# Kernel optimization log

Hardware: AMD Instinct MI355X
Metric: run time of the kernel (lower is better)

The kernel has to match this reference:

```python
import jax, jax.numpy as jnp
import numpy as np

B, S, D = 4, 2048, 1024
H, Dh = 16, 64


def setup_inputs() -> dict:
    key = jax.random.key(0)
    ks = jax.random.split(key, 9)
    s_in = 1.0 / np.sqrt(D)
    inp = {
        "key": jax.random.normal(ks[0], (B, S, D), jnp.float32),
        "value": jax.random.normal(ks[1], (B, S, D), jnp.float32),
        "query": jax.random.normal(ks[2], (B, S, D), jnp.float32),
        # Linear weights stored as [in, out] (math-equivalent to torch W.T)
        "Wq": jax.random.uniform(ks[3], (D, H * Dh), jnp.float32, -s_in, s_in),
        "bq": jax.random.uniform(ks[4], (H * Dh,), jnp.float32, -s_in, s_in),
        "Wk": jax.random.uniform(ks[5], (D, H * Dh), jnp.float32, -s_in, s_in),
        "bk": jax.random.uniform(ks[6], (H * Dh,), jnp.float32, -s_in, s_in),
        "Wv": jax.random.uniform(ks[7], (D, H * Dh), jnp.float32, -s_in, s_in),
        "bv": jax.random.uniform(ks[8], (H * Dh,), jnp.float32, -s_in, s_in),
    }
    return inp


def reference(key, value, query, Wq, bq, Wk, bk, Wv, bv):
    b, s, _ = key.shape
    # projections -> [B, H, S, Dh]
    q = (query @ Wq + bq).reshape(b, s, H, Dh).transpose(0, 2, 1, 3)
    k = (key @ Wk + bk).reshape(b, s, H, Dh).transpose(0, 2, 1, 3)
    v = (value @ Wv + bv).reshape(b, s, H, Dh).transpose(0, 2, 1, 3)
    scores = jnp.einsum("bhqd,bhkd->bhqk", q, k) / np.sqrt(Dh).astype(np.float32)
    p = jax.nn.softmax(scores, axis=-1)
    out = jnp.einsum("bhqk,bhkd->bhqd", p, v)  # [B, H, S, Dh]
    return out.transpose(0, 2, 1, 3).reshape(b, s, H * Dh)
```

## Files before the change

### kernel.cpp

```cpp
#include <hip/hip_runtime.h>

typedef __bf16 bf16;
typedef __bf16 bf16x8 __attribute__((ext_vector_type(8)));
typedef __bf16 bf16x4 __attribute__((ext_vector_type(4)));
typedef _Float16 f16x4 __attribute__((ext_vector_type(4)));
typedef _Float16 f16x8 __attribute__((ext_vector_type(8)));
typedef float  f32x4  __attribute__((ext_vector_type(4)));

#define LOG2E 1.44269504088896340736f

__device__ __forceinline__ void async16(const void* g, void* l) {
  __builtin_amdgcn_global_load_lds(
      (const __attribute__((address_space(1))) unsigned int*)g,
      (__attribute__((address_space(3))) unsigned int*)l, 16, 0, 0);
}

__device__ __forceinline__ f32x4 mfma_bf16(bf16x8 a, bf16x8 b, f32x4 c) {
  return __builtin_amdgcn_mfma_f32_16x16x32_bf16(a, b, c, 0, 0, 0);
}
__device__ __forceinline__ f32x4 mfma_f16k16(f16x4 a, f16x4 b, f32x4 c) {
  return __builtin_amdgcn_mfma_f32_16x16x16f16(a, b, c, 0, 0, 0);
}

__global__ __launch_bounds__(256) void cvt_f32_bf16(const float* __restrict__ in,
                                                    bf16* __restrict__ out) {
  int i = blockIdx.x * 256 + threadIdx.x;
  const float4* p = (const float4*)in;
  float4 a = p[i * 2], c = p[i * 2 + 1];
  bf16x8 r;
  r[0] = (bf16)a.x; r[1] = (bf16)a.y; r[2] = (bf16)a.z; r[3] = (bf16)a.w;
  r[4] = (bf16)c.x; r[5] = (bf16)c.y; r[6] = (bf16)c.z; r[7] = (bf16)c.w;
  ((bf16x8*)out)[i] = r;
}

__global__ __launch_bounds__(256) void wtrans(const float* __restrict__ W0,
                                              const float* __restrict__ W1,
                                              const float* __restrict__ W2,
                                              bf16* __restrict__ Wt) {
  const float* W = blockIdx.z == 0 ? W0 : (blockIdx.z == 1 ? W1 : W2);
  bf16* O = Wt + (size_t)blockIdx.z * (1024 * 1024);
  __shared__ float t[64 * 69];
  int tid = threadIdx.x;
  int k0 = blockIdx.x * 64, n0 = blockIdx.y * 64;
  int r0 = tid >> 4, c0 = (tid & 15) * 4;
#pragma unroll
  for (int rr = 0; rr < 4; rr++) {
    int k = r0 + rr * 16;
    float4 v = *(const float4*)(W + (k0 + k) * 1024 + n0 + c0);
    t[k * 69 + c0 + 0] = v.x; t[k * 69 + c0 + 1] = v.y;
    t[k * 69 + c0 + 2] = v.z; t[k * 69 + c0 + 3] = v.w;
  }
  __syncthreads();
#pragma unroll
  for (int rr = 0; rr < 4; rr++) {
    int n = r0 + rr * 16;
    bf16x4 o;
#pragma unroll
    for (int j = 0; j < 4; j++) o[j] = (bf16)t[(c0 + j) * 69 + n];
    *(bf16x4*)(O + (n0 + n) * 1024 + k0 + c0) = o;
  }
}

__global__ __launch_bounds__(256) void gemm_proj(const bf16* __restrict__ A,
                                                 const bf16* __restrict__ Bt,
                                                 const float* __restrict__ bias,
                                                 bf16* __restrict__ OutN,
                                                 _Float16* __restrict__ OutT,
                                                 int transV) {
  __shared__ bf16 smem[16384];
  bf16* sA = smem;
  bf16* sB = smem + 8192;
  const int tid = threadIdx.x;
  const int wave = tid >> 6, lane = tid & 63;
  const int quad = lane >> 4, l15 = lane & 15;
  const int m0 = blockIdx.x * 128, n0 = blockIdx.y * 128;

  const bf16* ap[4]; const bf16* bp[4]; int lo[4];
#pragma unroll
  for (int i = 0; i < 4; i++) {
    int g = wave * 256 + i * 64 + lane;
    int row = g >> 3, jl = (g & 7) ^ (row & 7);
    ap[i] = A + (m0 + row) * 1024 + jl * 8;
    bp[i] = Bt + (n0 + row) * 1024 + jl * 8;
    lo[i] = (wave * 256 + i * 64) * 8;
  }
  const int wm = (wave & 1) * 64, wn = (wave >> 1) * 64;
  f32x4 acc[4][4] = {};

  for (int kt = 0; kt < 16; kt++) {
    const int ko = kt * 64;
#pragma unroll
    for (int i = 0; i < 4; i++) async16(ap[i] + ko, sA + lo[i]);
#pragma unroll
    for (int i = 0; i < 4; i++) async16(bp[i] + ko, sB + lo[i]);
    __syncthreads();
#pragma unroll
    for (int ks = 0; ks < 2; ks++) {
      bf16x8 af[4], bv[4];
#pragma unroll
      for (int mt = 0; mt < 4; mt++) {
        int m = wm + mt * 16 + l15;
        int ph = (ks * 4 + quad) ^ (m & 7);
        af[mt] = *(const bf16x8*)(sA + m * 64 + ph * 8);
      }
#pragma unroll
      for (int nt = 0; nt < 4; nt++) {
        int n = wn + nt * 16 + l15;
        int ph = (ks * 4 + quad) ^ (n & 7);
        bv[nt] = *(const bf16x8*)(sB + n * 64 + ph * 8);
      }
#pragma unroll
      for (int mt = 0; mt < 4; mt++)
#pragma unroll
        for (int nt = 0; nt < 4; nt++)
          acc[mt][nt] = mfma_bf16(af[mt], bv[nt], acc[mt][nt]);
    }
    __syncthreads();
  }

  if (!transV) {
#pragma unroll
    for (int nt = 0; nt < 4; nt++) {
      int n = n0 + wn + nt * 16 + l15;
      float bc = bias[n];
#pragma unroll
      for (int mt = 0; mt < 4; mt++)
#pragma unroll
        for (int r = 0; r < 4; r++) {
          int m = m0 + wm + mt * 16 + quad * 4 + r;
          OutN[m * 1024 + n] = (bf16)(acc[mt][nt][r] + bc);
        }
    }
  } else {
    _Float16* sT = (_Float16*)smem;
    const int b = m0 >> 11, s0 = m0 & 2047;
    for (int half_ = 0; half_ < 2; half_++) {
      __syncthreads();
      if ((wave & 1) == half_) {
#pragma unroll
        for (int nt = 0; nt < 4; nt++) {
          int nl = wn + nt * 16 + l15;
          float bc = bias[n0 + nl];
#pragma unroll
          for (int mt = 0; mt < 4; mt++) {
            f16x4 pk;
#pragma unroll
            for (int r = 0; r < 4; r++) pk[r] = (_Float16)(acc[mt][nt][r] + bc);
            *(f16x4*)(sT + nl * 72 + mt * 16 + quad * 4) = pk;
          }
        }
      }
      __syncthreads();
      int nl = tid >> 1, mc = (tid & 1) * 32;
      int ng = n0 + nl, hh = ng >> 6, d = ng & 63;
      int base = ((b * 16 + hh) * 64 + d) * 2048 + s0 + half_ * 64 + mc;
#pragma unroll
      for (int j = 0; j < 4; j++) {
        f16x8 v = *(const f16x8*)(sT + nl * 72 + mc + j * 8);
        *(f16x8*)(OutT + base + j * 8) = v;
      }
    }
  }
}

__global__ __launch_bounds__(256) void attn(const bf16* __restrict__ Q,
                                            const bf16* __restrict__ K,
                                            const _Float16* __restrict__ Vt,
                                            float* __restrict__ Out) {
  __shared__ bf16 sQ[8192];
  __shared__ bf16 sK[4096];
  __shared__ _Float16 sV[4096];
  const int tid = threadIdx.x;
  const int wave = tid >> 6, lane = tid & 63;
  const int quad = lane >> 4, l15 = lane & 15;
  const int q0 = blockIdx.x * 128, h = blockIdx.y, b = blockIdx.z;
  const float SC = 0.125f * LOG2E;
  const bf16* Kbase = K + b * 2048 * 1024 + h * 64;
  const _Float16* Vbase = Vt + ((b * 16 + h) * 64) * 2048;

#pragma unroll
  for (int i = 0; i < 4; i++) {
    int g = i * 256 + tid;
    int row = g >> 3, jl = (g & 7) ^ (row & 7);
    async16(Q + (b * 2048 + q0 + row) * 1024 + h * 64 + jl * 8, sQ + g * 8);
  }
#pragma unroll
  for (int i = 0; i < 2; i++) {
    int g = i * 256 + tid;
    int row = g >> 3, jl = (g & 7) ^ (row & 7);
    async16(Kbase + row * 1024 + jl * 8, sK + g * 8);
    async16(Vbase + row * 2048 + jl * 8, sV + g * 8);
  }
  __syncthreads();

  bf16x8 qf[2][2];
#pragma unroll
  for (int qt2 = 0; qt2 < 2; qt2++)
#pragma unroll
    for (int ks = 0; ks < 2; ks++) {
      int m = wave * 32 + qt2 * 16 + l15;
      int ph = (ks * 4 + quad) ^ (m & 7);
      qf[qt2][ks] = *(const bf16x8*)(sQ + m * 64 + ph * 8);
    }

  f32x4 oaccT[2][4] = {};
  float ls[2] = {0.f, 0.f};

  for (int kv = 0; kv < 2048; kv += 64) {
#pragma unroll
    for (int t = 0; t < 4; t++) {
      int row = t * 16 + l15;
      bf16x8 kf0 = *(const bf16x8*)(sK + row * 64 + ((0 + quad) ^ (row & 7)) * 8);
      bf16x8 kf1 = *(const bf16x8*)(sK + row * 64 + ((4 + quad) ^ (row & 7)) * 8);
      f32x4 st0 = {}, st1 = {};
      st0 = mfma_bf16(kf0, qf[0][0], st0);
      st0 = mfma_bf16(kf1, qf[0][1], st0);
      st1 = mfma_bf16(kf0, qf[1][0], st1);
      st1 = mfma_bf16(kf1, qf[1][1], st1);
      f16x4 pf0, pf1;
#pragma unroll
      for (int r = 0; r < 4; r++) {
        float p0 = __builtin_amdgcn_exp2f(st0[r] * SC);
        float p1 = __builtin_amdgcn_exp2f(st1[r] * SC);
        ls[0] += p0; ls[1] += p1;
        pf0[r] = (_Float16)p0; pf1[r] = (_Float16)p1;
      }
      int gk = t * 2 + (quad >> 1), ofs = (quad & 1) * 4;
#pragma unroll
      for (int dt = 0; dt < 4; dt++) {
        int d = dt * 16 + l15;
        f16x4 va = *(const f16x4*)(sV + d * 64 + (gk ^ (d & 7)) * 8 + ofs);
        oaccT[0][dt] = mfma_f16k16(va, pf0, oaccT[0][dt]);
        oaccT[1][dt] = mfma_f16k16(va, pf1, oaccT[1][dt]);
      }
    }
    __syncthreads();
    if (kv + 64 < 2048) {
      int kn = kv + 64;
#pragma unroll
      for (int i = 0; i < 2; i++) {
        int g = i * 256 + tid;
        int row = g >> 3, jl = (g & 7) ^ (row & 7);
        async16(Kbase + (kn + row) * 1024 + jl * 8, sK + g * 8);
        async16(Vbase + row * 2048 + kn + jl * 8, sV + g * 8);
      }
      __syncthreads();
    }
  }

#pragma unroll
  for (int qt2 = 0; qt2 < 2; qt2++) {
    float l = ls[qt2];
    l += __shfl_xor(l, 16);
    l += __shfl_xor(l, 32);
    float inv = 1.f / l;
    int qrow = b * 2048 + q0 + wave * 32 + qt2 * 16 + l15;
#pragma unroll
    for (int dt = 0; dt < 4; dt++) {
      float4 v;
      v.x = oaccT[qt2][dt][0] * inv;
      v.y = oaccT[qt2][dt][1] * inv;
      v.z = oaccT[qt2][dt][2] * inv;
      v.w = oaccT[qt2][dt][3] * inv;
      *(float4*)(Out + qrow * 1024 + h * 64 + dt * 16 + quad * 4) = v;
    }
  }
}

extern "C" void kernel_launch(void* const* d_in, const int* in_sizes, int n_in,
                              void* d_out, int out_size, void* d_ws, size_t ws_size,
                              hipStream_t stream) {
  const float* key   = (const float*)d_in[0];
  const float* value = (const float*)d_in[1];
  const float* query = (const float*)d_in[2];
  const float* Wq = (const float*)d_in[3];
  const float* bq = (const float*)d_in[4];
  const float* Wk = (const float*)d_in[5];
  const float* bk = (const float*)d_in[6];
  const float* Wv = (const float*)d_in[7];
  const float* bv = (const float*)d_in[8];
  float* out = (float*)d_out;

  char* ws = (char*)d_ws;
  bf16* actb = (bf16*)(ws);
  bf16* wt   = (bf16*)(ws + 16777216);
  bf16* qo   = (bf16*)(ws + 16777216 + 6291456);
  bf16* ko   = (bf16*)(ws + 16777216 + 6291456 + 16777216);
  _Float16* vt = (_Float16*)(ws + 16777216 + 6291456 + 33554432);
  (void)in_sizes; (void)n_in; (void)out_size; (void)ws_size;

  wtrans<<<dim3(16, 16, 3), 256, 0, stream>>>(Wq, Wk, Wv, wt);

  cvt_f32_bf16<<<4096, 256, 0, stream>>>(query, actb);
  gemm_proj<<<dim3(64, 8), 256, 0, stream>>>(actb, wt, bq, qo, (_Float16*)nullptr, 0);

  cvt_f32_bf16<<<4096, 256, 0, stream>>>(key, actb);
  gemm_proj<<<dim3(64, 8), 256, 0, stream>>>(actb, wt + 1048576, bk, ko, (_Float16*)nullptr, 0);

  cvt_f32_bf16<<<4096, 256, 0, stream>>>(value, actb);
  gemm_proj<<<dim3(64, 8), 256, 0, stream>>>(actb, wt + 2097152, bv, (bf16*)nullptr, vt, 1);

  attn<<<dim3(16, 16, 4), 256, 0, stream>>>(qo, ko, vt, out);
}
```

Before: 331.0 us.

## Batch QKV projections, pre-swizzle V fragments, fold softmax scale, double-buffer attention loads

```diff
diff --git a/kernel.cpp b/kernel.cpp
--- a/kernel.cpp
+++ b/kernel.cpp
@@ -4,10 +4,10 @@
 typedef __bf16 bf16x8 __attribute__((ext_vector_type(8)));
 typedef __bf16 bf16x4 __attribute__((ext_vector_type(4)));
 typedef _Float16 f16x4 __attribute__((ext_vector_type(4)));
-typedef _Float16 f16x8 __attribute__((ext_vector_type(8)));
 typedef float  f32x4  __attribute__((ext_vector_type(4)));
 
 #define LOG2E 1.44269504088896340736f
+#define SCQ (0.125f * LOG2E)
 
 __device__ __forceinline__ void async16(const void* g, void* l) {
   __builtin_amdgcn_global_load_lds(
@@ -22,15 +22,20 @@
   return __builtin_amdgcn_mfma_f32_16x16x16f16(a, b, c, 0, 0, 0);
 }
 
-__global__ __launch_bounds__(256) void cvt_f32_bf16(const float* __restrict__ in,
-                                                    bf16* __restrict__ out) {
+__global__ __launch_bounds__(256) void cvt3(const float* __restrict__ q,
+                                            const float* __restrict__ k,
+                                            const float* __restrict__ v,
+                                            bf16* __restrict__ out) {
+  int z = blockIdx.y;
+  const float* in = z == 0 ? q : (z == 1 ? k : v);
+  bf16* o = out + (size_t)z * 8388608;
   int i = blockIdx.x * 256 + threadIdx.x;
   const float4* p = (const float4*)in;
   float4 a = p[i * 2], c = p[i * 2 + 1];
   bf16x8 r;
   r[0] = (bf16)a.x; r[1] = (bf16)a.y; r[2] = (bf16)a.z; r[3] = (bf16)a.w;
   r[4] = (bf16)c.x; r[5] = (bf16)c.y; r[6] = (bf16)c.z; r[7] = (bf16)c.w;
-  ((bf16x8*)out)[i] = r;
+  ((bf16x8*)o)[i] = r;
 }
 
 __global__ __launch_bounds__(256) void wtrans(const float* __restrict__ W0,
@@ -61,19 +66,25 @@
   }
 }
 
-__global__ __launch_bounds__(256) void gemm_proj(const bf16* __restrict__ A,
-                                                 const bf16* __restrict__ Bt,
-                                                 const float* __restrict__ bias,
-                                                 bf16* __restrict__ OutN,
-                                                 _Float16* __restrict__ OutT,
-                                                 int transV) {
+__global__ __launch_bounds__(256) void gemm_qkv(const bf16* __restrict__ Act,
+                                                const bf16* __restrict__ Wt,
+                                                const float* __restrict__ b0,
+                                                const float* __restrict__ b1,
+                                                const float* __restrict__ b2,
+                                                bf16* __restrict__ qo,
+                                                bf16* __restrict__ ko,
+                                                _Float16* __restrict__ vf) {
   __shared__ bf16 smem[16384];
   bf16* sA = smem;
   bf16* sB = smem + 8192;
   const int tid = threadIdx.x;
   const int wave = tid >> 6, lane = tid & 63;
   const int quad = lane >> 4, l15 = lane & 15;
+  const int z = blockIdx.z;
   const int m0 = blockIdx.x * 128, n0 = blockIdx.y * 128;
+  const bf16* A = Act + (size_t)z * 8388608;
+  const bf16* Bt = Wt + (size_t)z * 1048576;
+  const float* bias = z == 0 ? b0 : (z == 1 ? b1 : b2);
 
   const bf16* ap[4]; const bf16* bp[4]; int lo[4];
 #pragma unroll
@@ -88,11 +99,11 @@
   f32x4 acc[4][4] = {};
 
   for (int kt = 0; kt < 16; kt++) {
-    const int ko = kt * 64;
-#pragma unroll
-    for (int i = 0; i < 4; i++) async16(ap[i] + ko, sA + lo[i]);
-#pragma unroll
-    for (int i = 0; i < 4; i++) async16(bp[i] + ko, sB + lo[i]);
+    const int ko_ = kt * 64;
+#pragma unroll
+    for (int i = 0; i < 4; i++) async16(ap[i] + ko_, sA + lo[i]);
+#pragma unroll
+    for (int i = 0; i < 4; i++) async16(bp[i] + ko_, sB + lo[i]);
     __syncthreads();
 #pragma unroll
     for (int ks = 0; ks < 2; ks++) {
@@ -118,7 +129,9 @@
     __syncthreads();
   }
 
-  if (!transV) {
+  if (z != 2) {
+    bf16* O = z == 0 ? qo : ko;
+    const float sc = z == 0 ? SCQ : 1.0f;
 #pragma unroll
     for (int nt = 0; nt < 4; nt++) {
       int n = n0 + wn + nt * 16 + l15;
@@ -128,36 +141,24 @@
 #pragma unroll
         for (int r = 0; r < 4; r++) {
           int m = m0 + wm + mt * 16 + quad * 4 + r;
-          OutN[m * 1024 + n] = (bf16)(acc[mt][nt][r] + bc);
+          O[m * 1024 + n] = (bf16)((acc[mt][nt][r] + bc) * sc);
         }
     }
   } else {
-    _Float16* sT = (_Float16*)smem;
     const int b = m0 >> 11, s0 = m0 & 2047;
-    for (int half_ = 0; half_ < 2; half_++) {
-      __syncthreads();
-      if ((wave & 1) == half_) {
-#pragma unroll
-        for (int nt = 0; nt < 4; nt++) {
-          int nl = wn + nt * 16 + l15;
-          float bc = bias[n0 + nl];
-#pragma unroll
-          for (int mt = 0; mt < 4; mt++) {
-            f16x4 pk;
-#pragma unroll
-            for (int r = 0; r < 4; r++) pk[r] = (_Float16)(acc[mt][nt][r] + bc);
-            *(f16x4*)(sT + nl * 72 + mt * 16 + quad * 4) = pk;
-          }
-        }
-      }
-      __syncthreads();
-      int nl = tid >> 1, mc = (tid & 1) * 32;
-      int ng = n0 + nl, hh = ng >> 6, d = ng & 63;
-      int base = ((b * 16 + hh) * 64 + d) * 2048 + s0 + half_ * 64 + mc;
-#pragma unroll
-      for (int j = 0; j < 4; j++) {
-        f16x8 v = *(const f16x8*)(sT + nl * 72 + mc + j * 8);
-        *(f16x8*)(OutT + base + j * 8) = v;
+    const int kvb = (s0 + wm) >> 6;
+#pragma unroll
+    for (int nt = 0; nt < 4; nt++) {
+      int nn = n0 + wn + nt * 16;
+      int h = nn >> 6, dt = (nn >> 4) & 3;
+      float bc = bias[nn + l15];
+#pragma unroll
+      for (int mt = 0; mt < 4; mt++) {
+        f16x4 pk;
+#pragma unroll
+        for (int r = 0; r < 4; r++) pk[r] = (_Float16)(acc[mt][nt][r] + bc);
+        size_t off = ((((size_t)(b * 16 + h) * 32 + kvb) * 16 + (mt * 4 + dt)) * 64 + lane) * 4;
+        *(f16x4*)(vf + off) = pk;
       }
     }
   }
@@ -165,31 +166,30 @@
 
 __global__ __launch_bounds__(256) void attn(const bf16* __restrict__ Q,
                                             const bf16* __restrict__ K,
-                                            const _Float16* __restrict__ Vt,
+                                            const _Float16* __restrict__ VF,
                                             float* __restrict__ Out) {
   __shared__ bf16 sQ[8192];
-  __shared__ bf16 sK[4096];
-  __shared__ _Float16 sV[4096];
+  __shared__ bf16 sK[2][4096];
+  __shared__ _Float16 sV[2][4096];
   const int tid = threadIdx.x;
   const int wave = tid >> 6, lane = tid & 63;
   const int quad = lane >> 4, l15 = lane & 15;
   const int q0 = blockIdx.x * 128, h = blockIdx.y, b = blockIdx.z;
-  const float SC = 0.125f * LOG2E;
-  const bf16* Kbase = K + b * 2048 * 1024 + h * 64;
-  const _Float16* Vbase = Vt + ((b * 16 + h) * 64) * 2048;
+  const bf16* Kbase = K + (size_t)(b * 2048) * 1024 + h * 64;
+  const _Float16* Vbase = VF + (size_t)(b * 16 + h) * 131072;
 
 #pragma unroll
   for (int i = 0; i < 4; i++) {
     int g = i * 256 + tid;
     int row = g >> 3, jl = (g & 7) ^ (row & 7);
-    async16(Q + (b * 2048 + q0 + row) * 1024 + h * 64 + jl * 8, sQ + g * 8);
+    async16(Q + (size_t)(b * 2048 + q0 + row) * 1024 + h * 64 + jl * 8, sQ + g * 8);
   }
 #pragma unroll
   for (int i = 0; i < 2; i++) {
     int g = i * 256 + tid;
     int row = g >> 3, jl = (g & 7) ^ (row & 7);
-    async16(Kbase + row * 1024 + jl * 8, sK + g * 8);
-    async16(Vbase + row * 2048 + jl * 8, sV + g * 8);
+    async16(Kbase + row * 1024 + jl * 8, sK[0] + g * 8);
+    async16(Vbase + g * 8, sV[0] + g * 8);
   }
   __syncthreads();
 
@@ -199,19 +199,34 @@
 #pragma unroll
     for (int ks = 0; ks < 2; ks++) {
       int m = wave * 32 + qt2 * 16 + l15;
-      int ph = (ks * 4 + quad) ^ (m & 7);
+      int ph = (ks * 4 + quad) ^ (l15 & 7);
       qf[qt2][ks] = *(const bf16x8*)(sQ + m * 64 + ph * 8);
     }
 
   f32x4 oaccT[2][4] = {};
   float ls[2] = {0.f, 0.f};
 
-  for (int kv = 0; kv < 2048; kv += 64) {
+  const int ph0 = quad ^ (l15 & 7), ph1 = (4 + quad) ^ (l15 & 7);
+
+  for (int kvb = 0; kvb < 32; kvb++) {
+    const int cur = kvb & 1;
+    if (kvb < 31) {
+      int kn = (kvb + 1) * 64;
+#pragma unroll
+      for (int i = 0; i < 2; i++) {
+        int g = i * 256 + tid;
+        int row = g >> 3, jl = (g & 7) ^ (row & 7);
+        async16(Kbase + (size_t)(kn + row) * 1024 + jl * 8, sK[cur ^ 1] + g * 8);
+        async16(Vbase + (kvb + 1) * 4096 + g * 8, sV[cur ^ 1] + g * 8);
+      }
+    }
+    const bf16* sKc = sK[cur];
+    const _Float16* sVc = sV[cur];
 #pragma unroll
     for (int t = 0; t < 4; t++) {
       int row = t * 16 + l15;
-      bf16x8 kf0 = *(const bf16x8*)(sK + row * 64 + ((0 + quad) ^ (row & 7)) * 8);
-      bf16x8 kf1 = *(const bf16x8*)(sK + row * 64 + ((4 + quad) ^ (row & 7)) * 8);
+      bf16x8 kf0 = *(const bf16x8*)(sKc + row * 64 + ph0 * 8);
+      bf16x8 kf1 = *(const bf16x8*)(sKc + row * 64 + ph1 * 8);
       f32x4 st0 = {}, st1 = {};
       st0 = mfma_bf16(kf0, qf[0][0], st0);
       st0 = mfma_bf16(kf1, qf[0][1], st0);
@@ -220,32 +235,19 @@
       f16x4 pf0, pf1;
 #pragma unroll
       for (int r = 0; r < 4; r++) {
-        float p0 = __builtin_amdgcn_exp2f(st0[r] * SC);
-        float p1 = __builtin_amdgcn_exp2f(st1[r] * SC);
+        float p0 = __builtin_amdgcn_exp2f(st0[r]);
+        float p1 = __builtin_amdgcn_exp2f(st1[r]);
         ls[0] += p0; ls[1] += p1;
         pf0[r] = (_Float16)p0; pf1[r] = (_Float16)p1;
       }
-      int gk = t * 2 + (quad >> 1), ofs = (quad & 1) * 4;
 #pragma unroll
       for (int dt = 0; dt < 4; dt++) {
-        int d = dt * 16 + l15;
-        f16x4 va = *(const f16x4*)(sV + d * 64 + (gk ^ (d & 7)) * 8 + ofs);
+        f16x4 va = *(const f16x4*)(sVc + ((t * 4 + dt) * 64 + lane) * 4);
         oaccT[0][dt] = mfma_f16k16(va, pf0, oaccT[0][dt]);
         oaccT[1][dt] = mfma_f16k16(va, pf1, oaccT[1][dt]);
       }
     }
     __syncthreads();
-    if (kv + 64 < 2048) {
-      int kn = kv + 64;
-#pragma unroll
-      for (int i = 0; i < 2; i++) {
-        int g = i * 256 + tid;
-        int row = g >> 3, jl = (g & 7) ^ (row & 7);
-        async16(Kbase + (kn + row) * 1024 + jl * 8, sK + g * 8);
-        async16(Vbase + row * 2048 + kn + jl * 8, sV + g * 8);
-      }
-      __syncthreads();
-    }
   }
 
 #pragma unroll
@@ -262,7 +264,7 @@
       v.y = oaccT[qt2][dt][1] * inv;
       v.z = oaccT[qt2][dt][2] * inv;
       v.w = oaccT[qt2][dt][3] * inv;
-      *(float4*)(Out + qrow * 1024 + h * 64 + dt * 16 + quad * 4) = v;
+      *(float4*)(Out + (size_t)qrow * 1024 + h * 64 + dt * 16 + quad * 4) = v;
     }
   }
 }
@@ -282,23 +284,15 @@
   float* out = (float*)d_out;
 
   char* ws = (char*)d_ws;
-  bf16* actb = (bf16*)(ws);
-  bf16* wt   = (bf16*)(ws + 16777216);
-  bf16* qo   = (bf16*)(ws + 16777216 + 6291456);
-  bf16* ko   = (bf16*)(ws + 16777216 + 6291456 + 16777216);
-  _Float16* vt = (_Float16*)(ws + 16777216 + 6291456 + 33554432);
+  bf16* actb   = (bf16*)(ws);
+  bf16* wt     = (bf16*)(ws + 50331648);
+  bf16* qo     = (bf16*)(ws + 56623104);
+  bf16* ko     = (bf16*)(ws + 73400320);
+  _Float16* vf = (_Float16*)(ws + 90177536);
   (void)in_sizes; (void)n_in; (void)out_size; (void)ws_size;
 
   wtrans<<<dim3(16, 16, 3), 256, 0, stream>>>(Wq, Wk, Wv, wt);
-
-  cvt_f32_bf16<<<4096, 256, 0, stream>>>(query, actb);
-  gemm_proj<<<dim3(64, 8), 256, 0, stream>>>(actb, wt, bq, qo, (_Float16*)nullptr, 0);
-
-  cvt_f32_bf16<<<4096, 256, 0, stream>>>(key, actb);
-  gemm_proj<<<dim3(64, 8), 256, 0, stream>>>(actb, wt + 1048576, bk, ko, (_Float16*)nullptr, 0);
-
-  cvt_f32_bf16<<<4096, 256, 0, stream>>>(value, actb);
-  gemm_proj<<<dim3(64, 8), 256, 0, stream>>>(actb, wt + 2097152, bv, (bf16*)nullptr, vt, 1);
-
-  attn<<<dim3(16, 16, 4), 256, 0, stream>>>(qo, ko, vt, out);
-}
+  cvt3<<<dim3(4096, 3), 256, 0, stream>>>(query, key, value, actb);
+  gemm_qkv<<<dim3(64, 8, 3), 256, 0, stream>>>(actb, wt, bq, bk, bv, qo, ko, vf);
+  attn<<<dim3(16, 16, 4), 256, 0, stream>>>(qo, ko, vf, out);
+}
```

Measured after the change: 335.6 us. About the same (+1.4%).
